# Optimization experiments

Measured on AMD Instinct MI355X. Metric: run time of the kernel, lower is better.

Reference implementation:

```python
import jax, jax.numpy as jnp
import numpy as np

N = 8192
INP_DIM = 512
OUT_DIM = 256


def setup_inputs() -> dict:
    key = jax.random.key(0)
    k1, k2, k3, k4, k5 = jax.random.split(key, 5)
    x = jax.random.normal(k1, (N, INP_DIM), dtype=jnp.float32)
    adj = jax.random.uniform(k2, (N, N), dtype=jnp.float32)  # threshold at 0.5 below
    # learned params: w ~ torch.rand(inp_dim, out_dim); Linear(out_dim, out_dim)
    w = jax.random.uniform(k3, (INP_DIM, OUT_DIM), dtype=jnp.float32)
    bound = 1.0 / np.sqrt(OUT_DIM)
    lin_w = jax.random.uniform(k4, (OUT_DIM, OUT_DIM), minval=-bound, maxval=bound, dtype=jnp.float32)
    lin_b = jax.random.uniform(k5, (OUT_DIM,), minval=-bound, maxval=bound, dtype=jnp.float32)
    return {"x": x, "adj": adj, "w": w, "lin_w": lin_w, "lin_b": lin_b}


def reference(x, adj, w, lin_w, lin_b):
    n = adj.shape[0]
    # A = binarize(adj) + I
    A = jnp.where(adj > 0.5, 1.0, 0.0) + jnp.eye(n, dtype=adj.dtype)
    # D is diagonal, so inverse().sqrt() == diag(1/sqrt(deg)); deg >= 1 from self-loops
    d_inv_sqrt = jax.lax.rsqrt(jnp.sum(A, axis=1))  # [N]
    # A_hat = D^{-1/2} A D^{-1/2} as row/col scaling (same math, O(N^2))
    A_hat = A * d_inv_sqrt[:, None] * d_inv_sqrt[None, :]
    # message passing + feature transform
    h = jax.nn.relu((A_hat @ x) @ w)           # [N, out_dim]
    return h @ lin_w.T + lin_b                  # Linear(out_dim, out_dim)
```

## Files before the change

### kernel.cpp

```cpp
#include <hip/hip_runtime.h>
#include <hip/hip_bf16.h>

typedef __attribute__((ext_vector_type(4))) float f32x4;
typedef __attribute__((ext_vector_type(8))) short s16x8;
typedef unsigned int uint;
typedef unsigned short ushort;
typedef unsigned long long u64;


__device__ inline ushort f2bf(float f) {
  union { float f; uint u; } v; v.f = f;
  uint r = (v.u + 0x7FFFu + ((v.u >> 16) & 1u)) >> 16;
  return (ushort)r;
}
__device__ inline float bf2f(ushort h) { union { uint u; float f; } v; v.u = ((uint)h) << 16; return v.f; }
__device__ inline uint pack2(float a, float b) { return (uint)f2bf(a) | ((uint)f2bf(b) << 16); }
__device__ inline int kappa(int j) {
  return (j & ~255) | ((j & 3) << 6) | (((j >> 7) & 1) << 5) | ((j >> 2) & 31);
}
__device__ inline int ikappa(int k) {
  return (k & ~255) | ((k >> 6) & 3) | (((k >> 5) & 1) << 7) | ((k & 31) << 2);
}

__global__ __launch_bounds__(256, 4) void k_pack(const float* __restrict__ adj,
                                                 const float* __restrict__ w,
                                                 const float* __restrict__ lw,
                                                 uint* __restrict__ bits,
                                                 float* __restrict__ dinv,
                                                 float* __restrict__ dk,
                                                 ushort* __restrict__ wT,
                                                 ushort* __restrict__ lwb) {
  const int t = threadIdx.x, lane = t & 63, wv = t >> 6;
  const int b = blockIdx.x;
  const int row = b * 4 + wv;
  const float4* src = (const float4*)(adj + (size_t)row * 8192) + lane;
  uint* dst = bits + (size_t)row * 256;
  float4 A[4], B[4], C[4];
#pragma unroll
  for (int j = 0; j < 4; ++j) A[j] = src[j * 64];
#pragma unroll
  for (int j = 0; j < 4; ++j) B[j] = src[256 + j * 64];
  int cnt = 0;
#pragma unroll
  for (int bt = 0; bt < 8; ++bt) {
    if (bt + 2 < 8) {
#pragma unroll
      for (int j = 0; j < 4; ++j) C[j] = src[(bt + 2) * 256 + j * 64];
    }
#pragma unroll
    for (int j = 0; j < 4; ++j) {
      u64 b0 = __ballot(A[j].x > 0.5f), b1 = __ballot(A[j].y > 0.5f);
      u64 b2 = __ballot(A[j].z > 0.5f), b3 = __ballot(A[j].w > 0.5f);
      cnt += __popcll(b0) + __popcll(b1) + __popcll(b2) + __popcll(b3);
      if ((lane & 31) == 0) {
        uint4 v = (lane == 0)
          ? make_uint4((uint)b0, (uint)(b0 >> 32), (uint)b1, (uint)(b1 >> 32))
          : make_uint4((uint)b2, (uint)(b2 >> 32), (uint)b3, (uint)(b3 >> 32));
        *(uint4*)(dst + (bt * 4 + j) * 8 + (lane >> 5) * 4) = v;
      }
    }
#pragma unroll
    for (int j = 0; j < 4; ++j) { A[j] = B[j]; B[j] = C[j]; }
  }
  if (lane == 0) {
    float d = rsqrtf((float)(cnt + 1));
    dinv[row] = d;
    dk[kappa(row)] = d;
  }
  if (b < 16) {
#pragma unroll
    for (int kk = 0; kk < 32; ++kk) {
      int k = b * 32 + kk;
      wT[(size_t)t * 512 + k] = f2bf(w[(size_t)k * 256 + t]);
    }
  } else if (b < 24) {
    const int b2 = b - 16;
    const float4* s = (const float4*)lw + b2 * 2048;
    uint2* d = (uint2*)lwb + b2 * 2048;
#pragma unroll
    for (int ii = 0; ii < 8; ++ii) {
      float4 v = s[ii * 256 + t];
      uint2 p; p.x = pack2(v.x, v.y); p.y = pack2(v.z, v.w);
      d[ii * 256 + t] = p;
    }
  }
}

__global__ __launch_bounds__(512) void k_xw(const float* __restrict__ x,
                                            const ushort* __restrict__ wT,
                                            const float* __restrict__ dk,
                                            ushort* __restrict__ PB,
                                            ushort* __restrict__ zRow) {
  __shared__ ushort xa[2][32 * 64];
  __shared__ ushort zs[32 * 264];
  const int b = blockIdx.x;
  const int bp = (b & 3) * 64 + (b >> 2);
  const int t = threadIdx.x;
  const int lane = t & 63, wid = t >> 6;
  const int mg = wid >> 2, ng = wid & 3;
  const int rl = lane & 15, kg = lane >> 4;
  const int srow = t >> 4, sseg = t & 15;
  const int jrow = ((bp >> 3) << 8) + ((bp & 1) << 7) + ((bp >> 1) & 3) + srow * 4;
  const float4* xsrc = (const float4*)(x + (size_t)jrow * 512) + sseg;
  const int swb = (sseg * 8) ^ ((srow & 7) << 4);
  const int arow = mg * 16 + rl;
  float4 xv[8];
#pragma unroll
  for (int kc2 = 0; kc2 < 8; kc2++) xv[kc2] = xsrc[kc2 * 16];

  f32x4 acc[4];
#pragma unroll
  for (int q = 0; q < 4; q++) acc[q] = (f32x4){0.f, 0.f, 0.f, 0.f};

  {
    uint2 pk; pk.x = pack2(xv[0].x, xv[0].y); pk.y = pack2(xv[0].z, xv[0].w);
    *(uint2*)((char*)xa[0] + srow * 128 + swb) = pk;
  }
#pragma unroll
  for (int kc2 = 0; kc2 < 8; kc2++) {
    __syncthreads();
    if (kc2 < 7) {
      uint2 pk; pk.x = pack2(xv[kc2 + 1].x, xv[kc2 + 1].y);
      pk.y = pack2(xv[kc2 + 1].z, xv[kc2 + 1].w);
      *(uint2*)((char*)xa[(kc2 + 1) & 1] + srow * 128 + swb) = pk;
    }
#pragma unroll
    for (int ks = 0; ks < 2; ks++) {
      union { uint4 u; s16x8 s; } av;
      av.u = *(uint4*)((char*)xa[kc2 & 1] + arow * 128 + ((ks * 64 + kg * 16) ^ ((rl & 7) << 4)));
#pragma unroll
      for (int q = 0; q < 4; q++) {
        int n = ng * 64 + q * 16 + rl;
        union { uint4 u; s16x8 s; } bv;
        bv.u = *(const uint4*)(wT + (size_t)n * 512 + kc2 * 64 + ks * 32 + kg * 8);
        acc[q] = __builtin_amdgcn_mfma_f32_16x16x32_bf16(av.s, bv.s, acc[q], 0, 0, 0);
      }
    }
  }
  const int kb = bp * 32 + mg * 16 + kg * 4;
  float4 dk4 = *(const float4*)(dk + kb);
  const float dkv[4] = {dk4.x, dk4.y, dk4.z, dk4.w};
  char* pb0 = (char*)PB + (size_t)bp * 16384 + (mg * 2 + (kg >> 1)) * 256 + rl * 16 + (kg & 1) * 8;
  const int kk0 = mg * 16 + kg * 4;
#pragma unroll
  for (int q = 0; q < 4; q++) {
    int n = ng * 64 + q * 16 + rl;
    ushort zu[4];
#pragma unroll
    for (int r = 0; r < 4; r++) zu[r] = f2bf(acc[q][r] * dkv[r]);
    uint2 p;
    p.x = (uint)zu[0] | ((uint)zu[1] << 16);
    p.y = (uint)zu[2] | ((uint)zu[3] << 16);
    *(uint2*)(pb0 + (ng * 4 + q) * 1024) = p;
#pragma unroll
    for (int r = 0; r < 4; r++) zs[(kk0 + r) * 264 + n] = zu[r];
  }
  __syncthreads();
  {
    const int rr = t >> 4, seg = t & 15;
    uint4 v0 = *(uint4*)&zs[rr * 264 + seg * 16];
    uint4 v1 = *(uint4*)&zs[rr * 264 + seg * 16 + 8];
    ushort* dst = zRow + (size_t)ikappa(bp * 32 + rr) * 256 + seg * 16;
    *(uint4*)dst = v0;
    *(uint4*)(dst + 8) = v1;
  }
}

__global__ __launch_bounds__(512) void k_spmm(const uint* __restrict__ bits,
                                              const ushort* __restrict__ PB,
                                              ushort* __restrict__ part2) {
  __shared__ uint4 blds4[128 * 16];
  __shared__ uint2 lut[16];
  const int bx = blockIdx.x;
  const int kc = bx & 3, mb = bx >> 2;
  const int m0 = mb * 128;
  const int t = threadIdx.x;
  const int lane = t & 63, wid = t >> 6;
  const int mg = wid >> 2, ng = wid & 3;
  const int rl = lane & 15, kg = lane >> 4;
  if (t < 16) {
    uint2 e;
    e.x = ((t & 1u) ? 0x3F80u : 0u) | ((t & 2u) ? 0x3F800000u : 0u);
    e.y = ((t & 4u) ? 0x3F80u : 0u) | ((t & 8u) ? 0x3F800000u : 0u);
    lut[t] = e;
  }
  {
    const int r = t >> 2, p = t & 3;
    const uint4* src = (const uint4*)(bits + (size_t)(m0 + r) * 256 + kc * 64);
#pragma unroll
    for (int i = 0; i < 4; ++i) {
      int g = p * 4 + i;
      blds4[r * 16 + (g ^ (r & 15))] = src[g];
    }
  }
  const char* zb0 = (const char*)PB + (size_t)kc * 64 * 16384 + ng * 4096 + kg * 256 + rl * 16;
  __syncthreads();

  uint4 bufA[4], bufB[4];
#pragma unroll
  for (int q = 0; q < 4; ++q) bufA[q] = *(const uint4*)(zb0 + q * 1024);

  f32x4 acc[4][4];
#pragma unroll
  for (int f = 0; f < 4; ++f)
#pragma unroll
    for (int q = 0; q < 4; ++q) acc[f][q] = (f32x4){0.f, 0.f, 0.f, 0.f};

  int abase[4];
#pragma unroll
  for (int f = 0; f < 4; ++f) abase[f] = (mg * 64 + f * 16 + rl) * 16;
  const int axor = rl;
  const uint shft = kg * 8;

  for (int a = 0; a < 16; ++a) {
    uint4 aw[4];
#pragma unroll
    for (int f = 0; f < 4; ++f) aw[f] = blds4[abase[f] + (a ^ axor)];
#pragma unroll
    for (int s = 0; s < 4; ++s) {
      const int ks = a * 4 + s;
      const uint4* use = (s & 1) ? bufB : bufA;
      uint4* nxt = (s & 1) ? bufA : bufB;
      if (ks < 63) {
#pragma unroll
        for (int q = 0; q < 4; ++q)
          nxt[q] = *(const uint4*)(zb0 + (size_t)(ks + 1) * 16384 + q * 1024);
      }
#pragma unroll
      for (int f = 0; f < 4; ++f) {
        uint wrd = (s == 0) ? aw[f].x : (s == 1) ? aw[f].y : (s == 2) ? aw[f].z : aw[f].w;
        uint byt = (wrd >> shft) & 0xFFu;
        uint2 lo = lut[byt & 0xFu];
        uint2 hi = lut[byt >> 4];
        union { uint4 u; s16x8 s8; } au;
        au.u = make_uint4(lo.x, lo.y, hi.x, hi.y);
#pragma unroll
        for (int q = 0; q < 4; ++q) {
          union { uint4 u; s16x8 s8; } bu; bu.u = use[q];
          acc[f][q] = __builtin_amdgcn_mfma_f32_16x16x32_bf16(au.s8, bu.s8, acc[f][q], 0, 0, 0);
        }
      }
    }
  }
#pragma unroll
  for (int f = 0; f < 4; ++f)
#pragma unroll
    for (int q = 0; q < 4; ++q) {
      int n = ng * 64 + q * 16 + rl;
      int mt = mb * 4 + mg * 2 + (f >> 1);
      int moff = (f & 1) * 16 + kg * 4;
      uint2 p;
      p.x = pack2(acc[f][q][0], acc[f][q][1]);
      p.y = pack2(acc[f][q][2], acc[f][q][3]);
      *(uint2*)(part2 + ((((size_t)mt * 4 + kc) * 256 + n) * 32 + moff)) = p;
    }
}

__global__ __launch_bounds__(512) void k_lin(const ushort* __restrict__ part2,
                                             const ushort* __restrict__ zRow,
                                             const float* __restrict__ dinv,
                                             const ushort* __restrict__ lwb,
                                             const float* __restrict__ lb,
                                             float* __restrict__ out) {
  __shared__ ushort hA[32 * 256];
  __shared__ float sdinv[32];
  const int m0 = blockIdx.x * 32;
  const int t = threadIdx.x;
  if (t < 32) sdinv[t] = dinv[m0 + t];
  {
    const int n = t & 255, mh = t >> 8;
    float sum[16];
#pragma unroll
    for (int j = 0; j < 16; ++j)
      sum[j] = bf2f(zRow[(size_t)(m0 + mh * 16 + j) * 256 + n]);
#pragma unroll
    for (int kcp = 0; kcp < 4; kcp++) {
      const ushort* pp = part2 + (((size_t)blockIdx.x * 4 + kcp) * 256 + n) * 32 + mh * 16;
      uint4 pa = *(const uint4*)pp, pbq = *(const uint4*)(pp + 8);
      uint pu[8] = {pa.x, pa.y, pa.z, pa.w, pbq.x, pbq.y, pbq.z, pbq.w};
#pragma unroll
      for (int i = 0; i < 8; i++) {
        sum[2 * i]     += bf2f((ushort)(pu[i] & 0xFFFF));
        sum[2 * i + 1] += bf2f((ushort)(pu[i] >> 16));
      }
    }
    __syncthreads();
#pragma unroll
    for (int j = 0; j < 16; j++) {
      int m = mh * 16 + j;
      float h = sum[j] * sdinv[m];
      h = h > 0.f ? h : 0.f;
      *(ushort*)((char*)hA + m * 512 + ((n * 2) ^ ((m & 7) << 4))) = f2bf(h);
    }
  }
  __syncthreads();
  const int lane = t & 63, wid = t >> 6;
  const int rl = lane & 15, kg = lane >> 4;
  f32x4 acc[2][2];
#pragma unroll
  for (int f = 0; f < 2; f++)
#pragma unroll
    for (int q = 0; q < 2; q++) acc[f][q] = (f32x4){0.f, 0.f, 0.f, 0.f};

#pragma unroll
  for (int ks = 0; ks < 8; ks++) {
    union { uint4 u; s16x8 s; } av[2];
#pragma unroll
    for (int f = 0; f < 2; f++)
      av[f].u = *(uint4*)((char*)hA + (f * 16 + rl) * 512 + ((ks * 64 + kg * 16) ^ ((rl & 7) << 4)));
#pragma unroll
    for (int q = 0; q < 2; q++) {
      int no = wid * 32 + q * 16 + rl;
      union { uint4 u; s16x8 s; } bv;
      bv.u = *(const uint4*)(lwb + (size_t)no * 256 + ks * 32 + kg * 8);
#pragma unroll
      for (int f = 0; f < 2; f++)
        acc[f][q] = __builtin_amdgcn_mfma_f32_16x16x32_bf16(av[f].s, bv.s, acc[f][q], 0, 0, 0);
    }
  }
#pragma unroll
  for (int q = 0; q < 2; q++) {
    int no = wid * 32 + q * 16 + rl;
    float bb = lb[no];
#pragma unroll
    for (int f = 0; f < 2; f++) {
      int mbase = m0 + f * 16 + kg * 4;
#pragma unroll
      for (int r = 0; r < 4; r++)
        out[(size_t)(mbase + r) * 256 + no] = acc[f][q][r] + bb;
    }
  }
}

extern "C" void kernel_launch(void* const* d_in, const int* in_sizes, int n_in,
                              void* d_out, int out_size, void* d_ws, size_t ws_size,
                              hipStream_t stream) {
  const float* x   = (const float*)d_in[0];
  const float* adj = (const float*)d_in[1];
  const float* w   = (const float*)d_in[2];
  const float* lw  = (const float*)d_in[3];
  const float* lb  = (const float*)d_in[4];
  float* out = (float*)d_out;

  char* ws = (char*)d_ws;
  float*  dinv  = (float*)(ws + 0);
  float*  dk    = (float*)(ws + (32u << 10));
  ushort* lwb   = (ushort*)(ws + (128u << 10));
  ushort* wT    = (ushort*)(ws + (256u << 10));
  uint*   bits  = (uint*)(ws + (1ull << 20));
  ushort* PB    = (ushort*)(ws + (9ull << 20));
  ushort* part2 = (ushort*)(ws + (16ull << 20));
  ushort* zRow  = (ushort*)(ws + (48ull << 20));

  hipLaunchKernelGGL(k_pack, dim3(2048), dim3(256), 0, stream, adj, w, lw, bits, dinv, dk, wT, lwb);
  hipLaunchKernelGGL(k_xw, dim3(256), dim3(512), 0, stream, x, wT, dk, PB, zRow);
  hipLaunchKernelGGL(k_spmm, dim3(256), dim3(512), 0, stream, bits, PB, part2);
  hipLaunchKernelGGL(k_lin, dim3(256), dim3(512), 0, stream, part2, zRow, dinv, lwb, lb, out);
}
```

Measured before the change: 120.6 us.

## Fuse xw, spmm and linear kernels into one persistent kernel with grid barriers

Merges the three post-pack kernels into a single 256-block kernel that shares one LDS buffer and separates its phases with atomic-counter grid barriers instead of kernel boundaries. The aim is to remove two kernel launch gaps and tail drain between phases. It relies on all 256 blocks being co-resident (one block per CU on a 256-CU part), which would deadlock otherwise, and adds a memset launch to reset the counters.

```diff
diff --git a/kernel.cpp b/kernel.cpp
--- a/kernel.cpp
+++ b/kernel.cpp
@@ -20,6 +20,18 @@
 }
 __device__ inline int ikappa(int k) {
   return (k & ~255) | ((k >> 6) & 3) | (((k >> 5) & 1) << 7) | ((k & 31) << 2);
+}
+
+__device__ inline void gridbar(uint* ctr, int phase) {
+  __syncthreads();
+  if (threadIdx.x == 0) {
+    __threadfence();
+    __hip_atomic_fetch_add(&ctr[phase], 1u, __ATOMIC_ACQ_REL, __HIP_MEMORY_SCOPE_AGENT);
+    while (__hip_atomic_load(&ctr[phase], __ATOMIC_ACQUIRE, __HIP_MEMORY_SCOPE_AGENT) < 256u)
+      __builtin_amdgcn_s_sleep(2);
+    __threadfence();
+  }
+  __syncthreads();
 }
 
 __global__ __launch_bounds__(256, 4) void k_pack(const float* __restrict__ adj,
@@ -86,248 +98,245 @@
   }
 }
 
-__global__ __launch_bounds__(512) void k_xw(const float* __restrict__ x,
-                                            const ushort* __restrict__ wT,
-                                            const float* __restrict__ dk,
-                                            ushort* __restrict__ PB,
-                                            ushort* __restrict__ zRow) {
-  __shared__ ushort xa[2][32 * 64];
-  __shared__ ushort zs[32 * 264];
+__global__ __launch_bounds__(512, 1) void k_mega(
+    const float* __restrict__ x, const ushort* __restrict__ wT,
+    const float* __restrict__ dk, const float* __restrict__ dinv,
+    const uint* __restrict__ bits, const ushort* __restrict__ lwb,
+    const float* __restrict__ lb,
+    ushort* __restrict__ PB, ushort* __restrict__ zRow,
+    ushort* __restrict__ part2, float* __restrict__ out, uint* ctr) {
+  __shared__ __align__(16) char smem[33024];
+  __shared__ uint2 lut[16];
+  __shared__ float sdinv[32];
   const int b = blockIdx.x;
-  const int bp = (b & 3) * 64 + (b >> 2);
   const int t = threadIdx.x;
   const int lane = t & 63, wid = t >> 6;
-  const int mg = wid >> 2, ng = wid & 3;
   const int rl = lane & 15, kg = lane >> 4;
-  const int srow = t >> 4, sseg = t & 15;
-  const int jrow = ((bp >> 3) << 8) + ((bp & 1) << 7) + ((bp >> 1) & 3) + srow * 4;
-  const float4* xsrc = (const float4*)(x + (size_t)jrow * 512) + sseg;
-  const int swb = (sseg * 8) ^ ((srow & 7) << 4);
-  const int arow = mg * 16 + rl;
-  float4 xv[8];
-#pragma unroll
-  for (int kc2 = 0; kc2 < 8; kc2++) xv[kc2] = xsrc[kc2 * 16];
-
-  f32x4 acc[4];
-#pragma unroll
-  for (int q = 0; q < 4; q++) acc[q] = (f32x4){0.f, 0.f, 0.f, 0.f};
 
   {
-    uint2 pk; pk.x = pack2(xv[0].x, xv[0].y); pk.y = pack2(xv[0].z, xv[0].w);
-    *(uint2*)((char*)xa[0] + srow * 128 + swb) = pk;
-  }
-#pragma unroll
-  for (int kc2 = 0; kc2 < 8; kc2++) {
+    ushort* xa0 = (ushort*)smem;
+    ushort* xa1 = (ushort*)(smem + 4096);
+    ushort* zs  = (ushort*)(smem + 8192);
+    const int bp = (b & 3) * 64 + (b >> 2);
+    const int mg = wid >> 2, ng = wid & 3;
+    const int srow = t >> 4, sseg = t & 15;
+    const int jrow = ((bp >> 3) << 8) + ((bp & 1) << 7) + ((bp >> 1) & 3) + srow * 4;
+    const float4* xsrc = (const float4*)(x + (size_t)jrow * 512) + sseg;
+    const int swb = (sseg * 8) ^ ((srow & 7) << 4);
+    const int arow = mg * 16 + rl;
+    float4 xv[8];
+#pragma unroll
+    for (int kc2 = 0; kc2 < 8; kc2++) xv[kc2] = xsrc[kc2 * 16];
+
+    f32x4 acc[4];
+#pragma unroll
+    for (int q = 0; q < 4; q++) acc[q] = (f32x4){0.f, 0.f, 0.f, 0.f};
+
+    {
+      uint2 pk; pk.x = pack2(xv[0].x, xv[0].y); pk.y = pack2(xv[0].z, xv[0].w);
+      *(uint2*)((char*)xa0 + srow * 128 + swb) = pk;
+    }
+#pragma unroll
+    for (int kc2 = 0; kc2 < 8; kc2++) {
+      __syncthreads();
+      if (kc2 < 7) {
+        ushort* xan = (kc2 & 1) ? xa0 : xa1;
+        uint2 pk; pk.x = pack2(xv[kc2 + 1].x, xv[kc2 + 1].y);
+        pk.y = pack2(xv[kc2 + 1].z, xv[kc2 + 1].w);
+        *(uint2*)((char*)xan + srow * 128 + swb) = pk;
+      }
+      ushort* xac = (kc2 & 1) ? xa1 : xa0;
+#pragma unroll
+      for (int ks = 0; ks < 2; ks++) {
+        union { uint4 u; s16x8 s; } av;
+        av.u = *(uint4*)((char*)xac + arow * 128 + ((ks * 64 + kg * 16) ^ ((rl & 7) << 4)));
+#pragma unroll
+        for (int q = 0; q < 4; q++) {
+          int n = ng * 64 + q * 16 + rl;
+          union { uint4 u; s16x8 s; } bv;
+          bv.u = *(const uint4*)(wT + (size_t)n * 512 + kc2 * 64 + ks * 32 + kg * 8);
+          acc[q] = __builtin_amdgcn_mfma_f32_16x16x32_bf16(av.s, bv.s, acc[q], 0, 0, 0);
+        }
+      }
+    }
+    const int kb = bp * 32 + mg * 16 + kg * 4;
+    float4 dk4 = *(const float4*)(dk + kb);
+    const float dkv[4] = {dk4.x, dk4.y, dk4.z, dk4.w};
+    char* pb0 = (char*)PB + (size_t)bp * 16384 + (mg * 2 + (kg >> 1)) * 256 + rl * 16 + (kg & 1) * 8;
+    const int kk0 = mg * 16 + kg * 4;
+#pragma unroll
+    for (int q = 0; q < 4; q++) {
+      int n = ng * 64 + q * 16 + rl;
+      ushort zu[4];
+#pragma unroll
+      for (int r = 0; r < 4; r++) zu[r] = f2bf(acc[q][r] * dkv[r]);
+      uint2 p;
+      p.x = (uint)zu[0] | ((uint)zu[1] << 16);
+      p.y = (uint)zu[2] | ((uint)zu[3] << 16);
+      *(uint2*)(pb0 + (ng * 4 + q) * 1024) = p;
+#pragma unroll
+      for (int r = 0; r < 4; r++) zs[(kk0 + r) * 264 + n] = zu[r];
+    }
     __syncthreads();
-    if (kc2 < 7) {
-      uint2 pk; pk.x = pack2(xv[kc2 + 1].x, xv[kc2 + 1].y);
-      pk.y = pack2(xv[kc2 + 1].z, xv[kc2 + 1].w);
-      *(uint2*)((char*)xa[(kc2 + 1) & 1] + srow * 128 + swb) = pk;
-    }
-#pragma unroll
-    for (int ks = 0; ks < 2; ks++) {
-      union { uint4 u; s16x8 s; } av;
-      av.u = *(uint4*)((char*)xa[kc2 & 1] + arow * 128 + ((ks * 64 + kg * 16) ^ ((rl & 7) << 4)));
-#pragma unroll
-      for (int q = 0; q < 4; q++) {
+    {
+      const int rr = t >> 4, seg = t & 15;
+      uint4 v0 = *(uint4*)&zs[rr * 264 + seg * 16];
+      uint4 v1 = *(uint4*)&zs[rr * 264 + seg * 16 + 8];
+      ushort* dstz = zRow + (size_t)ikappa(bp * 32 + rr) * 256 + seg * 16;
+      *(uint4*)dstz = v0;
+      *(uint4*)(dstz + 8) = v1;
+    }
+  }
+  gridbar(ctr, 0);
+
+  {
+    uint4* blds4 = (uint4*)smem;
+    const int kc = b & 3, mb = b >> 2;
+    const int m0 = mb * 128;
+    const int mg = wid >> 2, ng = wid & 3;
+    if (t < 16) {
+      uint2 e;
+      e.x = ((t & 1u) ? 0x3F80u : 0u) | ((t & 2u) ? 0x3F800000u : 0u);
+      e.y = ((t & 4u) ? 0x3F80u : 0u) | ((t & 8u) ? 0x3F800000u : 0u);
+      lut[t] = e;
+    }
+    {
+      const int r = t >> 2, p = t & 3;
+      const uint4* src = (const uint4*)(bits + (size_t)(m0 + r) * 256 + kc * 64);
+#pragma unroll
+      for (int i = 0; i < 4; ++i) {
+        int g = p * 4 + i;
+        blds4[r * 16 + (g ^ (r & 15))] = src[g];
+      }
+    }
+    const char* zb0 = (const char*)PB + (size_t)kc * 64 * 16384 + ng * 4096 + kg * 256 + rl * 16;
+    __syncthreads();
+
+    uint4 bufA[4], bufB[4];
+#pragma unroll
+    for (int q = 0; q < 4; ++q) bufA[q] = *(const uint4*)(zb0 + q * 1024);
+
+    f32x4 acc[4][4];
+#pragma unroll
+    for (int f = 0; f < 4; ++f)
+#pragma unroll
+      for (int q = 0; q < 4; ++q) acc[f][q] = (f32x4){0.f, 0.f, 0.f, 0.f};
+
+    int abase[4];
+#pragma unroll
+    for (int f = 0; f < 4; ++f) abase[f] = (mg * 64 + f * 16 + rl) * 16;
+    const int axor = rl;
+    const uint shft = kg * 8;
+
+    for (int a = 0; a < 16; ++a) {
+      uint4 aw[4];
+#pragma unroll
+      for (int f = 0; f < 4; ++f) aw[f] = blds4[abase[f] + (a ^ axor)];
+#pragma unroll
+      for (int s = 0; s < 4; ++s) {
+        const int ks = a * 4 + s;
+        const uint4* use = (s & 1) ? bufB : bufA;
+        uint4* nxt = (s & 1) ? bufA : bufB;
+        if (ks < 63) {
+#pragma unroll
+          for (int q = 0; q < 4; ++q)
+            nxt[q] = *(const uint4*)(zb0 + (size_t)(ks + 1) * 16384 + q * 1024);
+        }
+#pragma unroll
+        for (int f = 0; f < 4; ++f) {
+          uint wrd = (s == 0) ? aw[f].x : (s == 1) ? aw[f].y : (s == 2) ? aw[f].z : aw[f].w;
+          uint byt = (wrd >> shft) & 0xFFu;
+          uint2 lo = lut[byt & 0xFu];
+          uint2 hi = lut[byt >> 4];
+          union { uint4 u; s16x8 s8; } au;
+          au.u = make_uint4(lo.x, lo.y, hi.x, hi.y);
+#pragma unroll
+          for (int q = 0; q < 4; ++q) {
+            union { uint4 u; s16x8 s8; } bu; bu.u = use[q];
+            acc[f][q] = __builtin_amdgcn_mfma_f32_16x16x32_bf16(au.s8, bu.s8, acc[f][q], 0, 0, 0);
+          }
+        }
+      }
+    }
+#pragma unroll
+    for (int f = 0; f < 4; ++f)
+#pragma unroll
+      for (int q = 0; q < 4; ++q) {
         int n = ng * 64 + q * 16 + rl;
+        int mt = mb * 4 + mg * 2 + (f >> 1);
+        int moff = (f & 1) * 16 + kg * 4;
+        uint2 p;
+        p.x = pack2(acc[f][q][0], acc[f][q][1]);
+        p.y = pack2(acc[f][q][2], acc[f][q][3]);
+        *(uint2*)(part2 + ((((size_t)mt * 4 + kc) * 256 + n) * 32 + moff)) = p;
+      }
+  }
+  gridbar(ctr, 1);
+
+  {
+    ushort* hA = (ushort*)smem;
+    const int m0 = b * 32;
+    if (t < 32) sdinv[t] = dinv[m0 + t];
+    {
+      const int n = t & 255, mh = t >> 8;
+      float sum[16];
+#pragma unroll
+      for (int j = 0; j < 16; ++j)
+        sum[j] = bf2f(zRow[(size_t)(m0 + mh * 16 + j) * 256 + n]);
+#pragma unroll
+      for (int kcp = 0; kcp < 4; kcp++) {
+        const ushort* pp = part2 + (((size_t)b * 4 + kcp) * 256 + n) * 32 + mh * 16;
+        uint4 pa = *(const uint4*)pp, pbq = *(const uint4*)(pp + 8);
+        uint pu[8] = {pa.x, pa.y, pa.z, pa.w, pbq.x, pbq.y, pbq.z, pbq.w};
+#pragma unroll
+        for (int i = 0; i < 8; i++) {
+          sum[2 * i]     += bf2f((ushort)(pu[i] & 0xFFFF));
+          sum[2 * i + 1] += bf2f((ushort)(pu[i] >> 16));
+        }
+      }
+      __syncthreads();
+#pragma unroll
+      for (int j = 0; j < 16; j++) {
+        int m = mh * 16 + j;
+        float h = sum[j] * sdinv[m];
+        h = h > 0.f ? h : 0.f;
+        *(ushort*)((char*)hA + m * 512 + ((n * 2) ^ ((m & 7) << 4))) = f2bf(h);
+      }
+    }
+    __syncthreads();
+    f32x4 acc[2][2];
+#pragma unroll
+    for (int f = 0; f < 2; f++)
+#pragma unroll
+      for (int q = 0; q < 2; q++) acc[f][q] = (f32x4){0.f, 0.f, 0.f, 0.f};
+
+#pragma unroll
+    for (int ks = 0; ks < 8; ks++) {
+      union { uint4 u; s16x8 s; } av[2];
+#pragma unroll
+      for (int f = 0; f < 2; f++)
+        av[f].u = *(uint4*)((char*)hA + (f * 16 + rl) * 512 + ((ks * 64 + kg * 16) ^ ((rl & 7) << 4)));
+#pragma unroll
+      for (int q = 0; q < 2; q++) {
+        int no = wid * 32 + q * 16 + rl;
         union { uint4 u; s16x8 s; } bv;
-        bv.u = *(const uint4*)(wT + (size_t)n * 512 + kc2 * 64 + ks * 32 + kg * 8);
-        acc[q] = __builtin_amdgcn_mfma_f32_16x16x32_bf16(av.s, bv.s, acc[q], 0, 0, 0);
-      }
-    }
-  }
-  const int kb = bp * 32 + mg * 16 + kg * 4;
-  float4 dk4 = *(const float4*)(dk + kb);
-  const float dkv[4] = {dk4.x, dk4.y, dk4.z, dk4.w};
-  char* pb0 = (char*)PB + (size_t)bp * 16384 + (mg * 2 + (kg >> 1)) * 256 + rl * 16 + (kg & 1) * 8;
-  const int kk0 = mg * 16 + kg * 4;
-#pragma unroll
-  for (int q = 0; q < 4; q++) {
-    int n = ng * 64 + q * 16 + rl;
-    ushort zu[4];
-#pragma unroll
-    for (int r = 0; r < 4; r++) zu[r] = f2bf(acc[q][r] * dkv[r]);
-    uint2 p;
-    p.x = (uint)zu[0] | ((uint)zu[1] << 16);
-    p.y = (uint)zu[2] | ((uint)zu[3] << 16);
-    *(uint2*)(pb0 + (ng * 4 + q) * 1024) = p;
-#pragma unroll
-    for (int r = 0; r < 4; r++) zs[(kk0 + r) * 264 + n] = zu[r];
-  }
-  __syncthreads();
-  {
-    const int rr = t >> 4, seg = t & 15;
-    uint4 v0 = *(uint4*)&zs[rr * 264 + seg * 16];
-    uint4 v1 = *(uint4*)&zs[rr * 264 + seg * 16 + 8];
-    ushort* dst = zRow + (size_t)ikappa(bp * 32 + rr) * 256 + seg * 16;
-    *(uint4*)dst = v0;
-    *(uint4*)(dst + 8) = v1;
-  }
-}
-
-__global__ __launch_bounds__(512) void k_spmm(const uint* __restrict__ bits,
-                                              const ushort* __restrict__ PB,
-                                              ushort* __restrict__ part2) {
-  __shared__ uint4 blds4[128 * 16];
-  __shared__ uint2 lut[16];
-  const int bx = blockIdx.x;
-  const int kc = bx & 3, mb = bx >> 2;
-  const int m0 = mb * 128;
-  const int t = threadIdx.x;
-  const int lane = t & 63, wid = t >> 6;
-  const int mg = wid >> 2, ng = wid & 3;
-  const int rl = lane & 15, kg = lane >> 4;
-  if (t < 16) {
-    uint2 e;
-    e.x = ((t & 1u) ? 0x3F80u : 0u) | ((t & 2u) ? 0x3F800000u : 0u);
-    e.y = ((t & 4u) ? 0x3F80u : 0u) | ((t & 8u) ? 0x3F800000u : 0u);
-    lut[t] = e;
-  }
-  {
-    const int r = t >> 2, p = t & 3;
-    const uint4* src = (const uint4*)(bits + (size_t)(m0 + r) * 256 + kc * 64);
-#pragma unroll
-    for (int i = 0; i < 4; ++i) {
-      int g = p * 4 + i;
-      blds4[r * 16 + (g ^ (r & 15))] = src[g];
-    }
-  }
-  const char* zb0 = (const char*)PB + (size_t)kc * 64 * 16384 + ng * 4096 + kg * 256 + rl * 16;
-  __syncthreads();
-
-  uint4 bufA[4], bufB[4];
-#pragma unroll
-  for (int q = 0; q < 4; ++q) bufA[q] = *(const uint4*)(zb0 + q * 1024);
-
-  f32x4 acc[4][4];
-#pragma unroll
-  for (int f = 0; f < 4; ++f)
-#pragma unroll
-    for (int q = 0; q < 4; ++q) acc[f][q] = (f32x4){0.f, 0.f, 0.f, 0.f};
-
-  int abase[4];
-#pragma unroll
-  for (int f = 0; f < 4; ++f) abase[f] = (mg * 64 + f * 16 + rl) * 16;
-  const int axor = rl;
-  const uint shft = kg * 8;
-
-  for (int a = 0; a < 16; ++a) {
-    uint4 aw[4];
-#pragma unroll
-    for (int f = 0; f < 4; ++f) aw[f] = blds4[abase[f] + (a ^ axor)];
-#pragma unroll
-    for (int s = 0; s < 4; ++s) {
-      const int ks = a * 4 + s;
-      const uint4* use = (s & 1) ? bufB : bufA;
-      uint4* nxt = (s & 1) ? bufA : bufB;
-      if (ks < 63) {
-#pragma unroll
-        for (int q = 0; q < 4; ++q)
-          nxt[q] = *(const uint4*)(zb0 + (size_t)(ks + 1) * 16384 + q * 1024);
-      }
-#pragma unroll
-      for (int f = 0; f < 4; ++f) {
-        uint wrd = (s == 0) ? aw[f].x : (s == 1) ? aw[f].y : (s == 2) ? aw[f].z : aw[f].w;
-        uint byt = (wrd >> shft) & 0xFFu;
-        uint2 lo = lut[byt & 0xFu];
-        uint2 hi = lut[byt >> 4];
-        union { uint4 u; s16x8 s8; } au;
-        au.u = make_uint4(lo.x, lo.y, hi.x, hi.y);
-#pragma unroll
-        for (int q = 0; q < 4; ++q) {
-          union { uint4 u; s16x8 s8; } bu; bu.u = use[q];
-          acc[f][q] = __builtin_amdgcn_mfma_f32_16x16x32_bf16(au.s8, bu.s8, acc[f][q], 0, 0, 0);
-        }
-      }
-    }
-  }
-#pragma unroll
-  for (int f = 0; f < 4; ++f)
-#pragma unroll
-    for (int q = 0; q < 4; ++q) {
-      int n = ng * 64 + q * 16 + rl;
-      int mt = mb * 4 + mg * 2 + (f >> 1);
-      int moff = (f & 1) * 16 + kg * 4;
-      uint2 p;
-      p.x = pack2(acc[f][q][0], acc[f][q][1]);
-      p.y = pack2(acc[f][q][2], acc[f][q][3]);
-      *(uint2*)(part2 + ((((size_t)mt * 4 + kc) * 256 + n) * 32 + moff)) = p;
-    }
-}
-
-__global__ __launch_bounds__(512) void k_lin(const ushort* __restrict__ part2,
-                                             const ushort* __restrict__ zRow,
-                                             const float* __restrict__ dinv,
-                                             const ushort* __restrict__ lwb,
-                                             const float* __restrict__ lb,
-                                             float* __restrict__ out) {
-  __shared__ ushort hA[32 * 256];
-  __shared__ float sdinv[32];
-  const int m0 = blockIdx.x * 32;
-  const int t = threadIdx.x;
-  if (t < 32) sdinv[t] = dinv[m0 + t];
-  {
-    const int n = t & 255, mh = t >> 8;
-    float sum[16];
-#pragma unroll
-    for (int j = 0; j < 16; ++j)
-      sum[j] = bf2f(zRow[(size_t)(m0 + mh * 16 + j) * 256 + n]);
-#pragma unroll
-    for (int kcp = 0; kcp < 4; kcp++) {
-      const ushort* pp = part2 + (((size_t)blockIdx.x * 4 + kcp) * 256 + n) * 32 + mh * 16;
-      uint4 pa = *(const uint4*)pp, pbq = *(const uint4*)(pp + 8);
-      uint pu[8] = {pa.x, pa.y, pa.z, pa.w, pbq.x, pbq.y, pbq.z, pbq.w};
-#pragma unroll
-      for (int i = 0; i < 8; i++) {
-        sum[2 * i]     += bf2f((ushort)(pu[i] & 0xFFFF));
-        sum[2 * i + 1] += bf2f((ushort)(pu[i] >> 16));
-      }
-    }
-    __syncthreads();
-#pragma unroll
-    for (int j = 0; j < 16; j++) {
-      int m = mh * 16 + j;
-      float h = sum[j] * sdinv[m];
-      h = h > 0.f ? h : 0.f;
-      *(ushort*)((char*)hA + m * 512 + ((n * 2) ^ ((m & 7) << 4))) = f2bf(h);
-    }
-  }
-  __syncthreads();
-  const int lane = t & 63, wid = t >> 6;
-  const int rl = lane & 15, kg = lane >> 4;
-  f32x4 acc[2][2];
-#pragma unroll
-  for (int f = 0; f < 2; f++)
-#pragma unroll
-    for (int q = 0; q < 2; q++) acc[f][q] = (f32x4){0.f, 0.f, 0.f, 0.f};
-
-#pragma unroll
-  for (int ks = 0; ks < 8; ks++) {
-    union { uint4 u; s16x8 s; } av[2];
-#pragma unroll
-    for (int f = 0; f < 2; f++)
-      av[f].u = *(uint4*)((char*)hA + (f * 16 + rl) * 512 + ((ks * 64 + kg * 16) ^ ((rl & 7) << 4)));
+        bv.u = *(const uint4*)(lwb + (size_t)no * 256 + ks * 32 + kg * 8);
+#pragma unroll
+        for (int f = 0; f < 2; f++)
+          acc[f][q] = __builtin_amdgcn_mfma_f32_16x16x32_bf16(av[f].s, bv.s, acc[f][q], 0, 0, 0);
+      }
+    }
 #pragma unroll
     for (int q = 0; q < 2; q++) {
       int no = wid * 32 + q * 16 + rl;
-      union { uint4 u; s16x8 s; } bv;
-      bv.u = *(const uint4*)(lwb + (size_t)no * 256 + ks * 32 + kg * 8);
-#pragma unroll
-      for (int f = 0; f < 2; f++)
-        acc[f][q] = __builtin_amdgcn_mfma_f32_16x16x32_bf16(av[f].s, bv.s, acc[f][q], 0, 0, 0);
-    }
-  }
-#pragma unroll
-  for (int q = 0; q < 2; q++) {
-    int no = wid * 32 + q * 16 + rl;
-    float bb = lb[no];
-#pragma unroll
-    for (int f = 0; f < 2; f++) {
-      int mbase = m0 + f * 16 + kg * 4;
-#pragma unroll
-      for (int r = 0; r < 4; r++)
-        out[(size_t)(mbase + r) * 256 + no] = acc[f][q][r] + bb;
+      float bb = lb[no];
+#pragma unroll
+      for (int f = 0; f < 2; f++) {
+        int mbase = m0 + f * 16 + kg * 4;
+#pragma unroll
+        for (int r = 0; r < 4; r++)
+          out[(size_t)(mbase + r) * 256 + no] = acc[f][q][r] + bb;
+      }
     }
   }
 }
@@ -345,6 +354,7 @@
   char* ws = (char*)d_ws;
   float*  dinv  = (float*)(ws + 0);
   float*  dk    = (float*)(ws + (32u << 10));
+  uint*   ctr   = (uint*)(ws + (96u << 10));
   ushort* lwb   = (ushort*)(ws + (128u << 10));
   ushort* wT    = (ushort*)(ws + (256u << 10));
   uint*   bits  = (uint*)(ws + (1ull << 20));
@@ -352,8 +362,8 @@
   ushort* part2 = (ushort*)(ws + (16ull << 20));
   ushort* zRow  = (ushort*)(ws + (48ull << 20));
 
+  hipMemsetAsync(ctr, 0, 16, stream);
   hipLaunchKernelGGL(k_pack, dim3(2048), dim3(256), 0, stream, adj, w, lw, bits, dinv, dk, wT, lwb);
-  hipLaunchKernelGGL(k_xw, dim3(256), dim3(512), 0, stream, x, wT, dk, PB, zRow);
-  hipLaunchKernelGGL(k_spmm, dim3(256), dim3(512), 0, stream, bits, PB, part2);
-  hipLaunchKernelGGL(k_lin, dim3(256), dim3(512), 0, stream, part2, zRow, dinv, lwb, lb, out);
-}
+  hipLaunchKernelGGL(k_mega, dim3(256), dim3(512), 0, stream,
+                     x, wT, dk, dinv, bits, lwb, lb, PB, zRow, part2, out, ctr);
+}
```

Result: slower. 194.2 us (+61.1%).
